# Kernel optimization log

Hardware: AMD Instinct MI355X
Metric: run time of the kernel (lower is better)

The kernel has to match this reference:

```python
import jax, jax.numpy as jnp
import numpy as np

EMBED_DIM = 768
NUM_HEADS = 12
HEAD_DIM = EMBED_DIM // NUM_HEADS
SEQ_LEN = 196
NUM_CLASSES = 3
BATCH = 256


def setup_inputs() -> dict:
    key = jax.random.key(0)
    ks = jax.random.split(key, 7)
    s = 0.02
    return {
        "x": jax.random.normal(ks[0], (BATCH, SEQ_LEN * EMBED_DIM), dtype=jnp.float32),
        "qkv_w": jax.random.normal(ks[1], (EMBED_DIM, 3 * EMBED_DIM), dtype=jnp.float32) * s,
        "qkv_b": jax.random.normal(ks[2], (3 * EMBED_DIM,), dtype=jnp.float32) * s,
        "out_w": jax.random.normal(ks[3], (EMBED_DIM, EMBED_DIM), dtype=jnp.float32) * s,
        "out_b": jax.random.normal(ks[4], (EMBED_DIM,), dtype=jnp.float32) * s,
        "cls_w": jax.random.normal(ks[5], (SEQ_LEN * EMBED_DIM, NUM_CLASSES), dtype=jnp.float32) * s,
        "cls_b": jax.random.normal(ks[6], (NUM_CLASSES,), dtype=jnp.float32) * s,
    }


def reference(x, qkv_w, qkv_b, out_w, out_b, cls_w, cls_b):
    B = x.shape[0]
    # (B, S*E) -> (B, S, E)
    xt = x.reshape(B, SEQ_LEN, EMBED_DIM)
    # QKV projection: (B, S, 3E) -> (B, S, H, 3*hd)
    qkv = (xt @ qkv_w + qkv_b).reshape(B, SEQ_LEN, NUM_HEADS, 3 * HEAD_DIM)
    q, k, v = jnp.split(qkv, 3, axis=-1)  # each (B, S, H, hd)
    # NOTE: faithful to source — attention is over the HEADS axis (HxH per token),
    # because q @ k.transpose(-2,-1) acts on the last two dims of (B,S,H,hd).
    scale = 1.0 / (HEAD_DIM ** 0.5)
    scores = jnp.einsum("bsid,bsjd->bsij", q, k) * scale  # (B, S, H, H)
    attn = jax.nn.softmax(scores, axis=-1)
    out = jnp.einsum("bsij,bsjd->bsid", attn, v).reshape(B, SEQ_LEN, EMBED_DIM)
    out = out @ out_w + out_b                 # (B, S, E)
    out = out.reshape(B, SEQ_LEN * EMBED_DIM)  # flatten(1)
    return out @ cls_w + cls_b                # (B, num_classes)
```

## Files before the change

kernel.cpp:

```cpp
#include <hip/hip_runtime.h>

typedef _Float16 f16;
typedef _Float16 f16x8 __attribute__((ext_vector_type(8)));
typedef float f32x4 __attribute__((ext_vector_type(4)));

#define SEQ   196
#define EMB   768
#define NHEAD 12
#define HD    64
#define BATCH 256
#define TOK   (BATCH*SEQ)
#define QKVN  (3*EMB)
#define CLSK  (SEQ*EMB)

__global__ __launch_bounds__(256) void k_cvt8(const float* __restrict__ in,
                                              f16* __restrict__ out, int n8) {
  int i = blockIdx.x * 256 + threadIdx.x;
  if (i >= n8) return;
  const float4* p = (const float4*)in + (size_t)i * 2;
  float4 a = p[0], b = p[1];
  f16x8 o;
  o[0]=(f16)a.x; o[1]=(f16)a.y; o[2]=(f16)a.z; o[3]=(f16)a.w;
  o[4]=(f16)b.x; o[5]=(f16)b.y; o[6]=(f16)b.z; o[7]=(f16)b.w;
  *((f16x8*)out + i) = o;
}

__global__ __launch_bounds__(256) void k_transpose_cvt(const float* __restrict__ W,
                                                       f16* __restrict__ WT,
                                                       int K, int N) {
  __shared__ float tile[32][33];
  int n0 = blockIdx.x * 32, k0 = blockIdx.y * 32;
  int t = threadIdx.x, tx = t & 31, ty = t >> 5;
  #pragma unroll
  for (int i = 0; i < 4; ++i) {
    int r = ty + i * 8;
    tile[r][tx] = W[(size_t)(k0 + r) * N + n0 + tx];
  }
  __syncthreads();
  #pragma unroll
  for (int i = 0; i < 4; ++i) {
    int r = ty + i * 8;
    WT[(size_t)(n0 + r) * K + k0 + tx] = (f16)tile[tx][r];
  }
}

__global__ __launch_bounds__(256) void k_gemm_bias(
    const f16* __restrict__ A, const f16* __restrict__ Bm,
    const float* __restrict__ bias, f16* __restrict__ C,
    int M, int N, int K) {
  __shared__ f16 As[128 * 64];
  __shared__ f16 Bs[128 * 64];
  const int t = threadIdx.x;
  const int l = t & 63;
  const int w = t >> 6;
  const int wr = w >> 1, wc = w & 1;

  const int nwg = gridDim.x;
  const int orig = blockIdx.x;
  const int q = nwg >> 3, r8 = nwg & 7;
  const int xcd = orig & 7, seq = orig >> 3;
  const int base = xcd < r8 ? xcd * (q + 1) : r8 * (q + 1) + (xcd - r8) * q;
  const int wg = base + seq;
  const int NB = N >> 7;
  const int bm = wg / NB, bn = wg - bm * NB;

  const size_t rowA0 = (size_t)bm * 128, rowB0 = (size_t)bn * 128;

  f32x4 acc[4][4] = {};

  for (int k0 = 0; k0 < K; k0 += 64) {
    if (k0) __syncthreads();
    #pragma unroll
    for (int i = 0; i < 4; ++i) {
      int qq = i * 256 + t;
      int rr = qq >> 3, c = qq & 7;
      int cs = c ^ (rr & 7);
      const f16* ga = A  + (rowA0 + rr) * K + k0 + cs * 8;
      const f16* gb = Bm + (rowB0 + rr) * K + k0 + cs * 8;
      f16* la = As + (size_t)(i * 256 + w * 64) * 8;
      f16* lb = Bs + (size_t)(i * 256 + w * 64) * 8;
      __builtin_amdgcn_global_load_lds((const __attribute__((address_space(1))) void*)ga,
                                       (__attribute__((address_space(3))) void*)la, 16, 0, 0);
      __builtin_amdgcn_global_load_lds((const __attribute__((address_space(1))) void*)gb,
                                       (__attribute__((address_space(3))) void*)lb, 16, 0, 0);
    }
    __syncthreads();
    #pragma unroll
    for (int ks = 0; ks < 2; ++ks) {
      f16x8 av[4], bv[4];
      const int k8 = ks * 4 + (l >> 4);
      #pragma unroll
      for (int m = 0; m < 4; ++m) {
        int rr = wr * 64 + m * 16 + (l & 15);
        av[m] = *(const f16x8*)((const char*)As + rr * 128 + ((k8 ^ (rr & 7)) << 4));
      }
      #pragma unroll
      for (int n = 0; n < 4; ++n) {
        int rr = wc * 64 + n * 16 + (l & 15);
        bv[n] = *(const f16x8*)((const char*)Bs + rr * 128 + ((k8 ^ (rr & 7)) << 4));
      }
      #pragma unroll
      for (int m = 0; m < 4; ++m)
        #pragma unroll
        for (int n = 0; n < 4; ++n)
          acc[m][n] = __builtin_amdgcn_mfma_f32_16x16x32_f16(av[m], bv[n], acc[m][n], 0, 0, 0);
    }
  }
  #pragma unroll
  for (int n = 0; n < 4; ++n) {
    int gcol = bn * 128 + wc * 64 + n * 16 + (l & 15);
    float bs = bias[gcol];
    #pragma unroll
    for (int m = 0; m < 4; ++m) {
      int grow0 = bm * 128 + wr * 64 + m * 16 + (l >> 4) * 4;
      #pragma unroll
      for (int j = 0; j < 4; ++j)
        C[(size_t)(grow0 + j) * N + gcol] = (f16)(acc[m][n][j] + bs);
    }
  }
}

__global__ __launch_bounds__(64) void k_attn(const f16* __restrict__ qkv,
                                             f16* __restrict__ aout) {
  const int tok = blockIdx.x;
  const int l = threadIdx.x;
  __shared__ f16 row[QKVN];
  __shared__ float sc[144];
  __shared__ float aw[144];
  const uint2* src = (const uint2*)(qkv + (size_t)tok * QKVN);
  uint2* dst = (uint2*)row;
  #pragma unroll
  for (int i = 0; i < 9; ++i) dst[l + i * 64] = src[l + i * 64];
  __syncthreads();
  for (int p = l; p < 144; p += 64) {
    int i = p / 12, j = p - i * 12;
    const f16x8* q8 = (const f16x8*)(row + i * 192);
    const f16x8* k8 = (const f16x8*)(row + j * 192 + 64);
    float s = 0.f;
    #pragma unroll
    for (int d8 = 0; d8 < 8; ++d8) {
      f16x8 a = q8[d8], b = k8[d8];
      #pragma unroll
      for (int e = 0; e < 8; ++e) s += (float)a[e] * (float)b[e];
    }
    sc[p] = s * 0.125f;
  }
  __syncthreads();
  if (l < 12) {
    float m = -1e30f;
    #pragma unroll
    for (int j = 0; j < 12; ++j) m = fmaxf(m, sc[l * 12 + j]);
    float e[12], sum = 0.f;
    #pragma unroll
    for (int j = 0; j < 12; ++j) { e[j] = __expf(sc[l * 12 + j] - m); sum += e[j]; }
    float inv = 1.f / sum;
    #pragma unroll
    for (int j = 0; j < 12; ++j) aw[l * 12 + j] = e[j] * inv;
  }
  __syncthreads();
  float vv[12];
  #pragma unroll
  for (int j = 0; j < 12; ++j) vv[j] = (float)row[j * 192 + 128 + l];
  f16* op = aout + (size_t)tok * EMB;
  #pragma unroll
  for (int i = 0; i < 12; ++i) {
    float o = 0.f;
    #pragma unroll
    for (int j = 0; j < 12; ++j) o += aw[i * 12 + j] * vv[j];
    op[i * 64 + l] = (f16)o;
  }
}

__global__ __launch_bounds__(256) void k_cls(const f16* __restrict__ out2,
                                             const float* __restrict__ cls_w,
                                             const float* __restrict__ cls_b,
                                             float* __restrict__ logits) {
  const int b = blockIdx.x, t = threadIdx.x;
  const f16* r = out2 + (size_t)b * CLSK;
  float s0 = 0.f, s1 = 0.f, s2 = 0.f;
  for (int c8 = t; c8 < CLSK / 8; c8 += 256) {
    f16x8 v = *((const f16x8*)r + c8);
    float wv[24];
    const float4* wp = (const float4*)(cls_w + (size_t)c8 * 24);
    #pragma unroll
    for (int i = 0; i < 6; ++i) *(float4*)&wv[i * 4] = wp[i];
    #pragma unroll
    for (int e = 0; e < 8; ++e) {
      float f = (float)v[e];
      s0 += f * wv[e * 3 + 0];
      s1 += f * wv[e * 3 + 1];
      s2 += f * wv[e * 3 + 2];
    }
  }
  __shared__ float r0[256], r1[256], r2[256];
  r0[t] = s0; r1[t] = s1; r2[t] = s2;
  __syncthreads();
  for (int off = 128; off > 0; off >>= 1) {
    if (t < off) { r0[t] += r0[t + off]; r1[t] += r1[t + off]; r2[t] += r2[t + off]; }
    __syncthreads();
  }
  if (t == 0) {
    logits[b * 3 + 0] = r0[0] + cls_b[0];
    logits[b * 3 + 1] = r1[0] + cls_b[1];
    logits[b * 3 + 2] = r2[0] + cls_b[2];
  }
}

extern "C" void kernel_launch(void* const* d_in, const int* in_sizes, int n_in,
                              void* d_out, int out_size, void* d_ws, size_t ws_size,
                              hipStream_t stream) {
  (void)in_sizes; (void)n_in; (void)out_size;
  const float* x      = (const float*)d_in[0];
  const float* qkv_w  = (const float*)d_in[1];
  const float* qkv_b  = (const float*)d_in[2];
  const float* out_w  = (const float*)d_in[3];
  const float* out_b  = (const float*)d_in[4];
  const float* cls_w  = (const float*)d_in[5];
  const float* cls_b  = (const float*)d_in[6];
  float* logits = (float*)d_out;

  const size_t SZ_X16 = (size_t)TOK * EMB * 2;
  const size_t SZ_QKV = (size_t)TOK * QKVN * 2;
  const size_t SZ_QT  = (size_t)QKVN * EMB * 2;
  const size_t SZ_OT  = (size_t)EMB * EMB * 2;
  if (ws_size < SZ_X16 + SZ_QKV + SZ_QT + SZ_OT) return;

  char* ws = (char*)d_ws;
  f16* x16  = (f16*)ws;
  f16* qkvb = (f16*)(ws + SZ_X16);
  f16* qkvT = (f16*)(ws + SZ_X16 + SZ_QKV);
  f16* outT = (f16*)(ws + SZ_X16 + SZ_QKV + SZ_QT);
  f16* attno = x16;
  f16* out2  = qkvb;

  k_cvt8<<<dim3(TOK * EMB / 8 / 256), dim3(256), 0, stream>>>(x, x16, TOK * EMB / 8);
  k_transpose_cvt<<<dim3(QKVN / 32, EMB / 32), dim3(256), 0, stream>>>(qkv_w, qkvT, EMB, QKVN);
  k_transpose_cvt<<<dim3(EMB / 32, EMB / 32), dim3(256), 0, stream>>>(out_w, outT, EMB, EMB);
  k_gemm_bias<<<dim3((TOK / 128) * (QKVN / 128)), dim3(256), 0, stream>>>(x16, qkvT, qkv_b, qkvb, TOK, QKVN, EMB);
  k_attn<<<dim3(TOK), dim3(64), 0, stream>>>(qkvb, attno);
  k_gemm_bias<<<dim3((TOK / 128) * (EMB / 128)), dim3(256), 0, stream>>>(attno, outT, out_b, out2, TOK, EMB, EMB);
  k_cls<<<dim3(BATCH), dim3(256), 0, stream>>>(out2, cls_w, cls_b, logits);
}
```

Before: 462.4 us.

## Fold output projection into classifier weights to drop the second big GEMM

```diff
diff --git a/kernel.cpp b/kernel.cpp
--- a/kernel.cpp
+++ b/kernel.cpp
@@ -42,6 +42,34 @@
     int r = ty + i * 8;
     WT[(size_t)(n0 + r) * K + k0 + tx] = (f16)tile[tx][r];
   }
+}
+
+__global__ __launch_bounds__(256) void k_extract_cls(const float* __restrict__ cls_w,
+                                                     f16* __restrict__ cls16,
+                                                     float* __restrict__ zbias) {
+  int idx = blockIdx.x * 256 + threadIdx.x;
+  int r = idx / EMB, e = idx - r * EMB;
+  int c = r / SEQ, s = r - c * SEQ;
+  cls16[(size_t)r * EMB + e] = (f16)cls_w[((size_t)s * EMB + e) * 3 + c];
+  if (blockIdx.x == 0)
+    for (int i = threadIdx.x; i < EMB; i += 256) zbias[i] = 0.f;
+}
+
+__global__ __launch_bounds__(256) void k_const3(const float* __restrict__ out_b,
+                                                const float* __restrict__ cls_w,
+                                                const float* __restrict__ cls_b,
+                                                float* __restrict__ const3) {
+  int c = blockIdx.x, t = threadIdx.x;
+  float s = 0.f;
+  for (int i = t; i < CLSK; i += 256) s += out_b[i % EMB] * cls_w[(size_t)i * 3 + c];
+  __shared__ float red[256];
+  red[t] = s;
+  __syncthreads();
+  for (int off = 128; off > 0; off >>= 1) {
+    if (t < off) red[t] += red[t + off];
+    __syncthreads();
+  }
+  if (t == 0) const3[c] = red[0] + cls_b[c];
 }
 
 __global__ __launch_bounds__(256) void k_gemm_bias(
@@ -171,25 +199,25 @@
   }
 }
 
-__global__ __launch_bounds__(256) void k_cls(const f16* __restrict__ out2,
-                                             const float* __restrict__ cls_w,
-                                             const float* __restrict__ cls_b,
-                                             float* __restrict__ logits) {
+__global__ __launch_bounds__(256) void k_cls2(const f16* __restrict__ attno,
+                                              const f16* __restrict__ W2,
+                                              const float* __restrict__ const3,
+                                              float* __restrict__ logits) {
   const int b = blockIdx.x, t = threadIdx.x;
-  const f16* r = out2 + (size_t)b * CLSK;
+  const f16* r = attno + (size_t)b * CLSK;
+  const f16x8* w0 = (const f16x8*)W2;
+  const f16x8* w1 = (const f16x8*)(W2 + CLSK);
+  const f16x8* w2 = (const f16x8*)(W2 + 2 * CLSK);
   float s0 = 0.f, s1 = 0.f, s2 = 0.f;
   for (int c8 = t; c8 < CLSK / 8; c8 += 256) {
     f16x8 v = *((const f16x8*)r + c8);
-    float wv[24];
-    const float4* wp = (const float4*)(cls_w + (size_t)c8 * 24);
-    #pragma unroll
-    for (int i = 0; i < 6; ++i) *(float4*)&wv[i * 4] = wp[i];
+    f16x8 a0 = w0[c8], a1 = w1[c8], a2 = w2[c8];
     #pragma unroll
     for (int e = 0; e < 8; ++e) {
       float f = (float)v[e];
-      s0 += f * wv[e * 3 + 0];
-      s1 += f * wv[e * 3 + 1];
-      s2 += f * wv[e * 3 + 2];
+      s0 += f * (float)a0[e];
+      s1 += f * (float)a1[e];
+      s2 += f * (float)a2[e];
     }
   }
   __shared__ float r0[256], r1[256], r2[256];
@@ -200,9 +228,9 @@
     __syncthreads();
   }
   if (t == 0) {
-    logits[b * 3 + 0] = r0[0] + cls_b[0];
-    logits[b * 3 + 1] = r1[0] + cls_b[1];
-    logits[b * 3 + 2] = r2[0] + cls_b[2];
+    logits[b * 3 + 0] = r0[0] + const3[0];
+    logits[b * 3 + 1] = r1[0] + const3[1];
+    logits[b * 3 + 2] = r2[0] + const3[2];
   }
 }
 
@@ -226,18 +254,24 @@
   if (ws_size < SZ_X16 + SZ_QKV + SZ_QT + SZ_OT) return;
 
   char* ws = (char*)d_ws;
-  f16* x16  = (f16*)ws;
-  f16* qkvb = (f16*)(ws + SZ_X16);
-  f16* qkvT = (f16*)(ws + SZ_X16 + SZ_QKV);
-  f16* outT = (f16*)(ws + SZ_X16 + SZ_QKV + SZ_QT);
+  const size_t base2 = SZ_X16 + SZ_QKV;
+  f16* x16    = (f16*)ws;
+  f16* qkvb   = (f16*)(ws + SZ_X16);
+  f16* qkvT   = (f16*)(ws + base2);
+  f16* outw16 = (f16*)(ws + base2);
+  f16* cls16  = (f16*)(ws + base2 + 1179648);
+  f16* W2     = (f16*)(ws + base2 + 2162688);
+  float* zbias  = (float*)(ws + base2 + SZ_QT);
+  float* const3 = (float*)(ws + base2 + SZ_QT + 3072);
   f16* attno = x16;
-  f16* out2  = qkvb;
 
   k_cvt8<<<dim3(TOK * EMB / 8 / 256), dim3(256), 0, stream>>>(x, x16, TOK * EMB / 8);
   k_transpose_cvt<<<dim3(QKVN / 32, EMB / 32), dim3(256), 0, stream>>>(qkv_w, qkvT, EMB, QKVN);
-  k_transpose_cvt<<<dim3(EMB / 32, EMB / 32), dim3(256), 0, stream>>>(out_w, outT, EMB, EMB);
   k_gemm_bias<<<dim3((TOK / 128) * (QKVN / 128)), dim3(256), 0, stream>>>(x16, qkvT, qkv_b, qkvb, TOK, QKVN, EMB);
   k_attn<<<dim3(TOK), dim3(64), 0, stream>>>(qkvb, attno);
-  k_gemm_bias<<<dim3((TOK / 128) * (EMB / 128)), dim3(256), 0, stream>>>(attno, outT, out_b, out2, TOK, EMB, EMB);
-  k_cls<<<dim3(BATCH), dim3(256), 0, stream>>>(out2, cls_w, cls_b, logits);
-}
+  k_cvt8<<<dim3(EMB * EMB / 8 / 256), dim3(256), 0, stream>>>(out_w, outw16, EMB * EMB / 8);
+  k_extract_cls<<<dim3(588 * EMB / 256), dim3(256), 0, stream>>>(cls_w, cls16, zbias);
+  k_const3<<<dim3(3), dim3(256), 0, stream>>>(out_b, cls_w, cls_b, const3);
+  k_gemm_bias<<<dim3((640 / 128) * (EMB / 128)), dim3(256), 0, stream>>>(cls16, outw16, zbias, W2, 640, EMB, EMB);
+  k_cls2<<<dim3(BATCH), dim3(256), 0, stream>>>(attno, W2, const3, logits);
+}
```

Measured after the change: 543.2 us. 1.17x slower.
